# Optimization experiments

Hardware: AMD Instinct MI355X
Metric: run time of the kernel (lower is better)

Reference implementation:

```python
import jax, jax.numpy as jnp
import numpy as np

HIDDEN = 1024
NUM_HEADS = 16
HEAD_DIM = HIDDEN // NUM_HEADS
LOCAL_WINDOW = 64
GLOBAL_WINDOW = 256
NEG_INF = -1.0e9


def _strided_mask(seq_len: int) -> jnp.ndarray:
    # Faithful vectorization of the torch loop:
    #   mask[i, max(0,i-w//2):min(S,i+w//2)] = 1  -> band j in [i-32, i+32)
    #   mask[i, ::stride] = 1, stride = max(1, S // global_window)
    i = jnp.arange(seq_len)[:, None]
    j = jnp.arange(seq_len)[None, :]
    half = LOCAL_WINDOW // 2
    local = (j >= i - half) & (j < i + half)
    stride = max(1, seq_len // GLOBAL_WINDOW)
    strided = (j % stride) == 0
    return local | strided  # bool [S, S]


def setup_inputs() -> dict:
    key = jax.random.key(0)
    ks = jax.random.split(key, 11)
    B, S, H = 2, 2048, HIDDEN
    scale = 1.0 / np.sqrt(H)
    inp = {
        "query": jax.random.normal(ks[0], (B, S, H), dtype=jnp.float32),
        "key": jax.random.normal(ks[1], (B, S, H), dtype=jnp.float32),
        "value": jax.random.normal(ks[2], (B, S, H), dtype=jnp.float32),
        # nn.Linear weights are [out, in]; y = x @ W.T + b
        "Wq": jax.random.normal(ks[3], (H, H), dtype=jnp.float32) * scale,
        "bq": jnp.zeros((H,), dtype=jnp.float32),
        "Wk": jax.random.normal(ks[4], (H, H), dtype=jnp.float32) * scale,
        "bk": jnp.zeros((H,), dtype=jnp.float32),
        "Wv": jax.random.normal(ks[5], (H, H), dtype=jnp.float32) * scale,
        "bv": jnp.zeros((H,), dtype=jnp.float32),
        "Wo": jax.random.normal(ks[6], (H, H), dtype=jnp.float32) * scale,
        "bo": jnp.zeros((H,), dtype=jnp.float32),
    }
    return inp


def reference(query, key, value, Wq, bq, Wk, bk, Wv, bv, Wo, bo):
    B, S, H = query.shape
    nH, dH = NUM_HEADS, HEAD_DIM
    scale = 1.0 / np.sqrt(dH)

    def split_heads(x):  # [B,S,H] -> [B,nH,S,dH]
        return x.reshape(B, S, nH, dH).transpose(0, 2, 1, 3)

    Q = split_heads(query @ Wq.T + bq)
    K = split_heads(key @ Wk.T + bk)
    V = split_heads(value @ Wv.T + bv)

    scores = jnp.einsum("bhqd,bhkd->bhqk", Q, K) * scale
    mask = _strided_mask(S)[None, None, :, :]
    scores = jnp.where(mask, scores, NEG_INF)
    attn = jax.nn.softmax(scores, axis=-1)
    # dropout is identity in eval mode
    context = jnp.einsum("bhqk,bhkd->bhqd", attn, V)
    context = context.transpose(0, 2, 1, 3).reshape(B, S, H)
    output = context @ Wo.T + bo
    return output, attn
```

## Files before the change

### kernel.cpp

```cpp
#include <hip/hip_runtime.h>

typedef unsigned int uint;
typedef unsigned short ushort_t;
typedef __bf16 bf16x8 __attribute__((ext_vector_type(8)));
typedef float f32x4 __attribute__((ext_vector_type(4)));

__device__ __forceinline__ int imin(int a, int b){ return a<b?a:b; }
__device__ __forceinline__ int imax(int a, int b){ return a>b?a:b; }

__device__ __forceinline__ ushort_t f2b(float f){
  uint u = __builtin_bit_cast(uint, f);
  u += 0x7FFFu + ((u>>16)&1u);
  return (ushort_t)(u>>16);
}
__device__ __forceinline__ float b2f(ushort_t s){
  uint u = ((uint)s)<<16;
  return __builtin_bit_cast(float, u);
}
__device__ __forceinline__ f32x4 fz4(){ f32x4 z; z[0]=0.f; z[1]=0.f; z[2]=0.f; z[3]=0.f; return z; }

struct CJob { const float* src; ushort_t* dst; int nvec; };

__global__ __launch_bounds__(256) void convert_k(CJob j0, CJob j1, CJob j2,
                                                 CJob j3, CJob j4, CJob j5)
{
  CJob jb;
  switch (blockIdx.y){
    case 0: jb=j0; break; case 1: jb=j1; break; case 2: jb=j2; break;
    case 3: jb=j3; break; case 4: jb=j4; break; default: jb=j5; break;
  }
  int stride = gridDim.x*256;
  for (int i = blockIdx.x*256 + threadIdx.x; i < jb.nvec; i += stride){
    const float4* s = (const float4*)(jb.src + (size_t)i*8);
    float4 v0 = s[0], v1 = s[1];
    uint4 pk;
    pk.x = (uint)f2b(v0.x) | ((uint)f2b(v0.y)<<16);
    pk.y = (uint)f2b(v0.z) | ((uint)f2b(v0.w)<<16);
    pk.z = (uint)f2b(v1.x) | ((uint)f2b(v1.y)<<16);
    pk.w = (uint)f2b(v1.z) | ((uint)f2b(v1.w)<<16);
    *(uint4*)(jb.dst + (size_t)i*8) = pk;
  }
}

struct GArg { const ushort_t* A; const ushort_t* W; const float* bias; void* O; };

template<bool OBF16>
__global__ __launch_bounds__(256) void gemm_nt(GArg g0, GArg g1, GArg g2)
{
  GArg g = (blockIdx.z==0) ? g0 : ((blockIdx.z==1) ? g1 : g2);
  __shared__ ushort_t As[128*40];
  __shared__ ushort_t Bs[128*40];
  const int tid  = threadIdx.x;
  const int lane = tid & 63;
  const int w    = tid >> 6;
  const int ml   = lane & 15, quad = lane >> 4;
  const int m0 = blockIdx.y*128, n0 = blockIdx.x*128;
  const int wm = (w>>1)*64, wn = (w&1)*64;

  f32x4 acc[4][4];
  #pragma unroll
  for (int i=0;i<4;i++)
    #pragma unroll
    for (int j=0;j<4;j++) acc[i][j]=fz4();

  for (int kt=0; kt<32; ++kt){
    #pragma unroll
    for (int i=0;i<2;i++){
      int s   = tid + i*256;
      int row = s>>2, c = s&3;
      int kof = kt*32 + c*8;
      *(uint4*)&As[row*40 + c*8] = *(const uint4*)(g.A + (size_t)(m0+row)*1024 + kof);
      *(uint4*)&Bs[row*40 + c*8] = *(const uint4*)(g.W + (size_t)(n0+row)*1024 + kof);
    }
    __syncthreads();
    bf16x8 af[4], bfr[4];
    #pragma unroll
    for (int t4=0;t4<4;t4++)
      af[t4]  = __builtin_bit_cast(bf16x8, *(const uint4*)&As[(wm + t4*16 + ml)*40 + quad*8]);
    #pragma unroll
    for (int t4=0;t4<4;t4++)
      bfr[t4] = __builtin_bit_cast(bf16x8, *(const uint4*)&Bs[(wn + t4*16 + ml)*40 + quad*8]);
    #pragma unroll
    for (int ti=0;ti<4;ti++)
      #pragma unroll
      for (int tj=0;tj<4;tj++)
        acc[ti][tj] = __builtin_amdgcn_mfma_f32_16x16x32_bf16(af[ti], bfr[tj], acc[ti][tj], 0,0,0);
    __syncthreads();
  }
  #pragma unroll
  for (int tj=0;tj<4;tj++){
    int gcol = n0 + wn + tj*16 + ml;
    float bv = g.bias[gcol];
    #pragma unroll
    for (int ti=0;ti<4;ti++){
      int growb = m0 + wm + ti*16 + quad*4;
      #pragma unroll
      for (int r=0;r<4;r++){
        float val = acc[ti][tj][r] + bv;
        size_t off = (size_t)(growb + r)*1024 + gcol;
        if (OBF16) ((ushort_t*)g.O)[off] = f2b(val);
        else       ((float*)g.O)[off]    = val;
      }
    }
  }
}

#define SW2 360
__global__ __launch_bounds__(128) void attn_k(
    const ushort_t* Qb, const ushort_t* Kb, const ushort_t* Vb,
    ushort_t* Ctxb, float* attn_out)
{
  __shared__ ushort_t stash[32*SW2];
  __shared__ float invl[32];
  const int lane = threadIdx.x & 63;
  const int w    = threadIdx.x >> 6;
  const int ml   = lane & 15, quad = lane >> 4;
  const int tile = blockIdx.x, h = blockIdx.y, b = blockIdx.z;
  const int i0  = tile*32;
  const int jl0 = i0 - 32;
  const int rb  = 16*w;
  const size_t bh = (size_t)b*2048*1024 + (size_t)h*64;

  bf16x8 aq0, aq1;
  {
    const ushort_t* qp = Qb + bh + (size_t)(i0 + rb + ml)*1024 + quad*8;
    aq0 = __builtin_bit_cast(bf16x8, *(const uint4*)qp);
    aq1 = __builtin_bit_cast(bf16x8, *(const uint4*)(qp + 32));
  }
  float lsum[4] = {0.f,0.f,0.f,0.f};
  for (int c=0;c<22;c++){
    int j  = (c<16) ? (128*c + 8*ml) : (jl0 + 16*(c-16) + ml);
    int jc = imin(imax(j,0),2047);
    const ushort_t* kp = Kb + bh + (size_t)jc*1024 + quad*8;
    bf16x8 kb0 = __builtin_bit_cast(bf16x8, *(const uint4*)kp);
    bf16x8 kb1 = __builtin_bit_cast(bf16x8, *(const uint4*)(kp + 32));
    f32x4 sc = fz4();
    sc = __builtin_amdgcn_mfma_f32_16x16x32_bf16(aq0, kb0, sc, 0,0,0);
    sc = __builtin_amdgcn_mfma_f32_16x16x32_bf16(aq1, kb1, sc, 0,0,0);
    int slot = 16*c + ml;
    #pragma unroll
    for (int r=0;r<4;r++){
      int rl = rb + quad*4 + r;
      int i  = i0 + rl;
      bool valid = (c<16) ? true :
        ((j>=0) && (j<2048) && ((j&7)!=0) && (j >= i-32) && (j < i+32));
      float e = valid ? __expf(sc[r]*0.125f) : 0.f;
      ushort_t eb = f2b(e);
      lsum[r] += b2f(eb);
      stash[rl*SW2 + slot] = eb;
    }
  }
  #pragma unroll
  for (int off=1; off<16; off<<=1){
    #pragma unroll
    for (int r=0;r<4;r++) lsum[r] += __shfl_xor(lsum[r], off);
  }
  if (ml==0){
    #pragma unroll
    for (int r=0;r<4;r++) invl[rb + quad*4 + r] = 1.f / lsum[r];
  }

  const size_t arow = ((size_t)(b*16 + h))*2048;
  for (int it=0; it<128; ++it){
    int r     = rb + (it>>3);
    int inner = ((it&7)<<6) + lane;
    int j0    = inner*4;
    float inv  = invl[r];
    float sval = b2f(stash[r*SW2 + (inner>>1)]);
    int off    = j0 - jl0;
    int offc   = imin(imax(off,0),92);
    uint2 lvu  = *(const uint2*)&stash[r*SW2 + 256 + offc];
    bool lok = (off>=0) && (off<96);
    float lx = lok ? b2f((ushort_t)(lvu.x & 0xffffu)) : 0.f;
    float ly = lok ? b2f((ushort_t)(lvu.x >> 16))     : 0.f;
    float lz = lok ? b2f((ushort_t)(lvu.y & 0xffffu)) : 0.f;
    float lw = lok ? b2f((ushort_t)(lvu.y >> 16))     : 0.f;
    f32x4 o;
    o[0] = ((inner&1)==0) ? inv*sval : inv*lx;
    o[1] = inv*ly; o[2] = inv*lz; o[3] = inv*lw;
    __builtin_nontemporal_store(o, (f32x4*)&attn_out[(arow + i0 + r)*2048 + j0]);
  }

  f32x4 pacc[4];
  #pragma unroll
  for (int nt=0;nt<4;nt++) pacc[nt]=fz4();
  const ushort_t* prow = &stash[(rb + ml)*SW2];
  for (int ck=0; ck<11; ++ck){
    int s0 = ck*32;
    bf16x8 pa = __builtin_bit_cast(bf16x8, *(const uint4*)(prow + s0 + quad*8));
    ushort_t vr[4][8];
    #pragma unroll
    for (int e=0;e<8;e++){
      int s = s0 + quad*8 + e;
      int j = (s<256) ? 8*s : (jl0 + s - 256);
      int jc = imin(imax(j,0),2047);
      const ushort_t* vp = Vb + bh + (size_t)jc*1024 + ml;
      #pragma unroll
      for (int nt=0;nt<4;nt++) vr[nt][e] = vp[nt*16];
    }
    #pragma unroll
    for (int nt=0;nt<4;nt++){
      uint4 pk;
      pk.x = (uint)vr[nt][0] | ((uint)vr[nt][1]<<16);
      pk.y = (uint)vr[nt][2] | ((uint)vr[nt][3]<<16);
      pk.z = (uint)vr[nt][4] | ((uint)vr[nt][5]<<16);
      pk.w = (uint)vr[nt][6] | ((uint)vr[nt][7]<<16);
      bf16x8 bfr = __builtin_bit_cast(bf16x8, pk);
      pacc[nt] = __builtin_amdgcn_mfma_f32_16x16x32_bf16(pa, bfr, pacc[nt], 0,0,0);
    }
  }
  #pragma unroll
  for (int nt=0;nt<4;nt++){
    #pragma unroll
    for (int rr=0;rr<4;rr++){
      int r = rb + quad*4 + rr;
      float val = pacc[nt][rr] * invl[r];
      Ctxb[bh + (size_t)(i0 + r)*1024 + nt*16 + ml] = f2b(val);
    }
  }
}

extern "C" void kernel_launch(void* const* d_in, const int* in_sizes, int n_in,
                              void* d_out, int out_size, void* d_ws, size_t ws_size,
                              hipStream_t stream) {
  (void)in_sizes; (void)n_in; (void)out_size; (void)ws_size;
  const float* query = (const float*)d_in[0];
  const float* key_  = (const float*)d_in[1];
  const float* value = (const float*)d_in[2];
  const float* Wq = (const float*)d_in[3];
  const float* bq = (const float*)d_in[4];
  const float* Wk = (const float*)d_in[5];
  const float* bk = (const float*)d_in[6];
  const float* Wv = (const float*)d_in[7];
  const float* bv = (const float*)d_in[8];
  const float* Wo = (const float*)d_in[9];
  const float* bo = (const float*)d_in[10];

  char* ws = (char*)d_ws;
  ushort_t* Qb   = (ushort_t*)(ws);
  ushort_t* Kb   = (ushort_t*)(ws + (size_t)( 8<<20));
  ushort_t* Vb   = (ushort_t*)(ws + (size_t)(16<<20));
  ushort_t* Ctxb = (ushort_t*)(ws + (size_t)(24<<20));

  float* out = (float*)d_out;
  float* attn_out = out + (size_t)4096*1024;

  ushort_t* scr = (ushort_t*)attn_out;
  ushort_t* Aq  = scr;
  ushort_t* Ak  = scr + (size_t)1*4096*1024;
  ushort_t* Av  = scr + (size_t)2*4096*1024;
  ushort_t* Wqb = scr + (size_t)3*4096*1024;
  ushort_t* Wkb = Wqb + (size_t)1024*1024;
  ushort_t* Wvb = Wkb + (size_t)1024*1024;
  ushort_t* Wob = Qb;

  const int NA = 4096*1024/8;
  const int NW = 1024*1024/8;

  CJob ja{query, Aq, NA}, jb{key_, Ak, NA}, jc{value, Av, NA};
  CJob jd{Wq, Wqb, NW}, je{Wk, Wkb, NW}, jf{Wv, Wvb, NW};
  convert_k<<<dim3(1024,6), 256, 0, stream>>>(ja, jb, jc, jd, je, jf);

  GArg ga{Aq, Wqb, bq, Qb};
  GArg gb{Ak, Wkb, bk, Kb};
  GArg gc{Av, Wvb, bv, Vb};
  gemm_nt<true><<<dim3(8,32,3), 256, 0, stream>>>(ga, gb, gc);

  attn_k<<<dim3(64,16,2), 128, 0, stream>>>(Qb, Kb, Vb, Ctxb, attn_out);

  CJob jo{Wo, Wob, NW};
  convert_k<<<dim3(512,1), 256, 0, stream>>>(jo, jo, jo, jo, jo, jo);

  GArg go{Ctxb, Wob, bo, out};
  gemm_nt<false><<<dim3(8,32,1), 256, 0, stream>>>(go, go, go);
}
```

Before: 739.2 us.

## Use direct global-to-LDS loads with XOR swizzle and remap block IDs across XCDs

The GEMM tile loads now go straight from global memory into LDS through global_load_lds, skipping the register round trip. The LDS tile stride drops from a padded 40 to 32 elements, and an XOR swizzle replaces the padding to avoid bank conflicts. Block indices in both the GEMM and the attention kernel are remapped so that neighbouring tiles land on the same XCD, which should improve L2 reuse of shared K/W rows. The risks are that the swizzle must match exactly between the write and read patterns, and the remap assumes the grid sizes stay fixed.

Result: faster. 703.5 us (-4.8%).

```diff
diff --git a/kernel.cpp b/kernel.cpp
--- a/kernel.cpp
+++ b/kernel.cpp
@@ -18,6 +18,13 @@
   return __builtin_bit_cast(float, u);
 }
 __device__ __forceinline__ f32x4 fz4(){ f32x4 z; z[0]=0.f; z[1]=0.f; z[2]=0.f; z[3]=0.f; return z; }
+
+__device__ __forceinline__ void gload16(const void* g, void* lds){
+  __builtin_amdgcn_global_load_lds(
+      (const __attribute__((address_space(1))) void*)g,
+      (__attribute__((address_space(3))) void*)lds,
+      16, 0, 0);
+}
 
 struct CJob { const float* src; ushort_t* dst; int nvec; };
 
@@ -48,15 +55,25 @@
 __global__ __launch_bounds__(256) void gemm_nt(GArg g0, GArg g1, GArg g2)
 {
   GArg g = (blockIdx.z==0) ? g0 : ((blockIdx.z==1) ? g1 : g2);
-  __shared__ ushort_t As[128*40];
-  __shared__ ushort_t Bs[128*40];
+  __shared__ __align__(16) ushort_t As[128*32];
+  __shared__ __align__(16) ushort_t Bs[128*32];
   const int tid  = threadIdx.x;
   const int lane = tid & 63;
   const int w    = tid >> 6;
   const int ml   = lane & 15, quad = lane >> 4;
-  const int m0 = blockIdx.y*128, n0 = blockIdx.x*128;
+
+  int lid = blockIdx.x + 8*blockIdx.y;
+  int t   = (lid & 7)*32 + (lid >> 3);
+  const int m0 = (t >> 3)*128, n0 = (t & 7)*128;
   const int wm = (w>>1)*64, wn = (w&1)*64;
 
+  const int srow = lane >> 2;
+  const int scol = ((lane & 3) ^ ((lane >> 3) & 3))*8;
+  const int rA0 = w*16, rA1 = 64 + w*16;
+  const ushort_t* gA = g.A + (size_t)m0*1024;
+  const ushort_t* gB = g.W + (size_t)n0*1024;
+  const int sxor = (quad ^ ((ml >> 1) & 3))*8;
+
   f32x4 acc[4][4];
   #pragma unroll
   for (int i=0;i<4;i++)
@@ -64,22 +81,20 @@
     for (int j=0;j<4;j++) acc[i][j]=fz4();
 
   for (int kt=0; kt<32; ++kt){
-    #pragma unroll
-    for (int i=0;i<2;i++){
-      int s   = tid + i*256;
-      int row = s>>2, c = s&3;
-      int kof = kt*32 + c*8;
-      *(uint4*)&As[row*40 + c*8] = *(const uint4*)(g.A + (size_t)(m0+row)*1024 + kof);
-      *(uint4*)&Bs[row*40 + c*8] = *(const uint4*)(g.W + (size_t)(n0+row)*1024 + kof);
-    }
+    int kof = kt*32 + scol;
+    gload16(gA + (size_t)(rA0+srow)*1024 + kof, &As[rA0*32]);
+    gload16(gA + (size_t)(rA1+srow)*1024 + kof, &As[rA1*32]);
+    gload16(gB + (size_t)(rA0+srow)*1024 + kof, &Bs[rA0*32]);
+    gload16(gB + (size_t)(rA1+srow)*1024 + kof, &Bs[rA1*32]);
     __syncthreads();
+
     bf16x8 af[4], bfr[4];
     #pragma unroll
     for (int t4=0;t4<4;t4++)
-      af[t4]  = __builtin_bit_cast(bf16x8, *(const uint4*)&As[(wm + t4*16 + ml)*40 + quad*8]);
+      af[t4]  = __builtin_bit_cast(bf16x8, *(const uint4*)&As[(wm + t4*16 + ml)*32 + sxor]);
     #pragma unroll
     for (int t4=0;t4<4;t4++)
-      bfr[t4] = __builtin_bit_cast(bf16x8, *(const uint4*)&Bs[(wn + t4*16 + ml)*40 + quad*8]);
+      bfr[t4] = __builtin_bit_cast(bf16x8, *(const uint4*)&Bs[(wn + t4*16 + ml)*32 + sxor]);
     #pragma unroll
     for (int ti=0;ti<4;ti++)
       #pragma unroll
@@ -115,7 +130,9 @@
   const int lane = threadIdx.x & 63;
   const int w    = threadIdx.x >> 6;
   const int ml   = lane & 15, quad = lane >> 4;
-  const int tile = blockIdx.x, h = blockIdx.y, b = blockIdx.z;
+  int lid = blockIdx.x + 64*(blockIdx.y + 16*blockIdx.z);
+  int tt  = (lid & 7)*256 + (lid >> 3);
+  const int tile = tt & 63, h = (tt >> 6) & 15, b = tt >> 10;
   const int i0  = tile*32;
   const int jl0 = i0 - 32;
   const int rb  = 16*w;
```
